# Optimization experiments

Hardware: AMD Instinct MI355X
Metric: run time of the kernel (lower is better)

Reference implementation:

```python
import jax, jax.numpy as jnp
import numpy as np

OBS_LEN = 8
PRED_LEN = 12
BATCH = 65536
EMB = 64
H = 64


def setup_inputs() -> dict:
    key = jax.random.key(0)
    ks = jax.random.split(key, 18)
    s = 1.0 / np.sqrt(H)  # torch default uniform bound scale, used as std here

    def p(k, shape):
        return (jax.random.normal(k, shape, dtype=jnp.float32) * s).astype(jnp.float32)

    return {
        "obs_traj": jax.random.normal(ks[0], (OBS_LEN, BATCH, 2), dtype=jnp.float32),
        "obs_traj_rel": jax.random.normal(ks[1], (OBS_LEN, BATCH, 2), dtype=jnp.float32),
        # encoder params
        "enc_emb_w": p(ks[2], (EMB, 2)),
        "enc_emb_b": p(ks[3], (EMB,)),
        "enc_w_ih": p(ks[4], (4 * H, EMB)),
        "enc_w_hh": p(ks[5], (4 * H, H)),
        "enc_b_ih": p(ks[6], (4 * H,)),
        "enc_b_hh": p(ks[7], (4 * H,)),
        # decoder params
        "dec_emb_w": p(ks[8], (EMB, 2)),
        "dec_emb_b": p(ks[9], (EMB,)),
        "dec_w_ih": p(ks[10], (4 * H, EMB)),
        "dec_w_hh": p(ks[11], (4 * H, H)),
        "dec_b_ih": p(ks[12], (4 * H,)),
        "dec_b_hh": p(ks[13], (4 * H,)),
        "h2p_w": p(ks[14], (2, H)),
        "h2p_b": p(ks[15], (2,)),
    }


def _lstm_cell(h, c, x, w_ih, w_hh, b_ih, b_hh):
    # torch nn.LSTM gate order: i, f, g, o
    gates = x @ w_ih.T + h @ w_hh.T + (b_ih + b_hh)
    i, f, g, o = jnp.split(gates, 4, axis=-1)
    c_new = jax.nn.sigmoid(f) * c + jax.nn.sigmoid(i) * jnp.tanh(g)
    h_new = jax.nn.sigmoid(o) * jnp.tanh(c_new)
    return h_new, c_new


def reference(obs_traj, obs_traj_rel,
              enc_emb_w, enc_emb_b, enc_w_ih, enc_w_hh, enc_b_ih, enc_b_hh,
              dec_emb_w, dec_emb_b, dec_w_ih, dec_w_hh, dec_b_ih, dec_b_hh,
              h2p_w, h2p_b):
    batch = obs_traj_rel.shape[1]

    # ---------- Encoder ----------
    enc_in = obs_traj_rel @ enc_emb_w.T + enc_emb_b  # [T, B, EMB]

    def enc_step(carry, x_t):
        h, c = carry
        h, c = _lstm_cell(h, c, x_t, enc_w_ih, enc_w_hh, enc_b_ih, enc_b_hh)
        return (h, c), None

    h0 = jnp.zeros((batch, H), dtype=obs_traj_rel.dtype)
    c0 = jnp.zeros((batch, H), dtype=obs_traj_rel.dtype)
    (h_enc, _), _ = jax.lax.scan(enc_step, (h0, c0), enc_in)

    # ---------- Decoder ----------
    dec_h = h_enc                                   # final encoder hidden seeds decoder
    dec_c = jnp.zeros((batch, H), dtype=obs_traj_rel.dtype)
    last_pos_rel = obs_traj_rel[-1]
    dec_in = last_pos_rel @ dec_emb_w.T + dec_emb_b  # [B, EMB]

    def dec_step(carry, _):
        h, c, x = carry
        h, c = _lstm_cell(h, c, x, dec_w_ih, dec_w_hh, dec_b_ih, dec_b_hh)
        rel_pos = h @ h2p_w.T + h2p_b               # [B, 2]
        x_next = rel_pos @ dec_emb_w.T + dec_emb_b  # [B, EMB]
        return (h, c, x_next), rel_pos

    (_, _, _), pred_traj_fake_rel = jax.lax.scan(
        dec_step, (dec_h, dec_c, dec_in), None, length=PRED_LEN)
    return pred_traj_fake_rel  # [PRED_LEN, B, 2]
```

## Files before the change

### kernel.cpp

```cpp
#include <hip/hip_runtime.h>

#define OBS_LEN 8
#define PRED_LEN 12
#define TILE_B 32
#define NTHREADS 256

typedef __attribute__((ext_vector_type(8))) short short8;
typedef __attribute__((ext_vector_type(4))) float floatx4;
typedef __attribute__((ext_vector_type(2))) float floatx2;
typedef __attribute__((ext_vector_type(4))) unsigned short ushortx4;
typedef __attribute__((ext_vector_type(2))) unsigned int u32x2;
typedef unsigned short u16;
typedef unsigned int u32;

#define L2E 1.442695040888963f

__device__ __forceinline__ u16 f2bf(float f) {
  __bf16 b = (__bf16)f;
  return __builtin_bit_cast(u16, b);
}
__device__ __forceinline__ float bf2f(u16 h) {
  return __builtin_bit_cast(float, ((u32)h) << 16);
}
__device__ __forceinline__ float rndbf(float f) { return (float)(__bf16)f; }

#if __has_builtin(__builtin_amdgcn_exp2f)
__device__ __forceinline__ float fexp2_(float x) { return __builtin_amdgcn_exp2f(x); }
#else
__device__ __forceinline__ float fexp2_(float x) { return exp2f(x); }
#endif
__device__ __forceinline__ floatx2 exp2v(floatx2 x) {
  floatx2 r;
  r.x = fexp2_(x.x);
  r.y = fexp2_(x.y);
  return r;
}
#if __has_builtin(__builtin_amdgcn_rcpf)
__device__ __forceinline__ floatx2 rcp2(floatx2 x) {
  floatx2 r;
  r.x = __builtin_amdgcn_rcpf(x.x);
  r.y = __builtin_amdgcn_rcpf(x.y);
  return r;
}
#else
__device__ __forceinline__ floatx2 rcp2(floatx2 x) {
  return floatx2{1.0f / x.x, 1.0f / x.y};
}
#endif

__device__ __forceinline__ floatx4 mfma_bf(short8 a, short8 b, floatx4 c) {
  return __builtin_amdgcn_mfma_f32_16x16x32_bf16(a, b, c, 0, 0, 0);
}

__device__ __forceinline__ int swz(int s, int b) {
  return s * 64 + ((b ^ (s & 7)) * 8);
}

__device__ __forceinline__ void load_afrags(const float* __restrict__ W,
                                            short8 (&af)[4][2],
                                            int u0, int q, int l16) {
#pragma unroll
  for (int t = 0; t < 4; ++t)
#pragma unroll
    for (int kf = 0; kf < 2; ++kf) {
      const float* src = W + (t * 64 + u0 + l16) * 64 + kf * 32 + q * 8;
      const floatx4 w0 = *(const floatx4*)src;
      const floatx4 w1 = *(const floatx4*)(src + 4);
      short8 a;
#pragma unroll
      for (int j = 0; j < 4; ++j) {
        a[j] = (short)f2bf(w0[j]);
        a[j + 4] = (short)f2bf(w1[j]);
      }
      af[t][kf] = a;
    }
}

__device__ __forceinline__ void cell_step(const u16* __restrict__ rdh,
                                          const u16* __restrict__ rdx,
                                          u16* __restrict__ wrh,
                                          const short8 (&afh)[4][2],
                                          const short8 (&afx)[4][2],
                                          const float* __restrict__ biasrow,
                                          floatx2 (&c)[2][2],
                                          int q, int l16, int wv, int u0) {
#pragma unroll
  for (int n = 0; n < 2; ++n) {
    const int s = n * 16 + l16;
    const int sw = s & 7;
    const u16* hr = rdh + s * 64;
    const u16* xr = rdx + s * 64;
    const short8 hb0 = *(const short8*)(hr + ((q ^ sw) * 8));
    const short8 hb1 = *(const short8*)(hr + (((q + 4) ^ sw) * 8));
    const short8 xb0 = *(const short8*)(xr + ((q ^ sw) * 8));
    const short8 xb1 = *(const short8*)(xr + (((q + 4) ^ sw) * 8));
    floatx4 acc[4];
#pragma unroll
    for (int t = 0; t < 4; ++t) {
      const floatx4 bias = *(const floatx4*)(biasrow + t * 64 + u0 + q * 4);
      acc[t] = mfma_bf(afh[t][0], hb0, bias);
    }
#pragma unroll
    for (int t = 0; t < 4; ++t) acc[t] = mfma_bf(afx[t][0], xb0, acc[t]);
#pragma unroll
    for (int t = 0; t < 4; ++t) acc[t] = mfma_bf(afh[t][1], hb1, acc[t]);
#pragma unroll
    for (int t = 0; t < 4; ++t) acc[t] = mfma_bf(afx[t][1], xb1, acc[t]);
    u32 hpk[2];
#pragma unroll
    for (int p = 0; p < 2; ++p) {
      const floatx2 iv = {acc[0][2 * p], acc[0][2 * p + 1]};
      const floatx2 fv = {acc[1][2 * p], acc[1][2 * p + 1]};
      const floatx2 gv = {acc[2][2 * p], acc[2][2 * p + 1]};
      const floatx2 ov = {acc[3][2 * p], acc[3][2 * p + 1]};
      const floatx2 ei = exp2v(iv * -L2E);
      const floatx2 ef = exp2v(fv * -L2E);
      const floatx2 eg = exp2v(gv * (2.0f * L2E));
      const floatx2 eo = exp2v(ov * -L2E);
      const floatx2 A = ei + 1.0f;
      const floatx2 F = ef + 1.0f;
      const floatx2 Bg = eg + 1.0f;
      const floatx2 P = A * Bg;
      const floatx2 num = c[n][p] * P + (eg - 1.0f) * F;
      const floatx2 cn = num * rcp2(F * P);
      c[n][p] = cn;
      const floatx2 ec = exp2v(cn * (2.0f * L2E));
      const floatx2 h = (ec - 1.0f) * rcp2((eo + 1.0f) * (ec + 1.0f));
      hpk[p] = (u32)f2bf(h.x) | ((u32)f2bf(h.y) << 16);
    }
    *(u32x2*)(wrh + s * 64 + (((wv * 2 + (q >> 1)) ^ sw) * 8) + (q & 1) * 4) =
        u32x2{hpk[0], hpk[1]};
  }
}

__device__ __forceinline__ void xgen8(float rb0, float rb1,
                                      const float* __restrict__ ew0,
                                      const float* __restrict__ ew1,
                                      const float* __restrict__ eb,
                                      u16* __restrict__ xw, int s8, int p8) {
  short8 v;
#pragma unroll
  for (int j = 0; j < 8; ++j) {
    const int e = p8 * 8 + j;
    v[j] = (short)f2bf(rb0 * ew0[e] + (rb1 * ew1[e] + eb[e]));
  }
  *(short8*)(xw + swz(s8, p8)) = v;
}

__device__ __forceinline__ void areldot(const u16* __restrict__ h,
                                        const floatx2* __restrict__ hwp,
                                        float b2p0, float b2p1, int s8, int p8,
                                        float& r0, float& r1) {
  const short8 hv = *(const short8*)(h + swz(s8, p8));
  floatx2 d = {0.f, 0.f};
#pragma unroll
  for (int j = 0; j < 8; ++j) d = hwp[p8 * 8 + j] * bf2f((u16)hv[j]) + d;
  d.x += __shfl_xor(d.x, 1);
  d.x += __shfl_xor(d.x, 2);
  d.x += __shfl_xor(d.x, 4);
  d.y += __shfl_xor(d.y, 1);
  d.y += __shfl_xor(d.y, 2);
  d.y += __shfl_xor(d.y, 4);
  r0 = d.x + b2p0;
  r1 = d.y + b2p1;
}

__global__ void __launch_bounds__(NTHREADS, 3)
lstm_kernel(const float* __restrict__ obs_rel,
            const float* __restrict__ enc_emb_w, const float* __restrict__ enc_emb_b,
            const float* __restrict__ enc_w_ih, const float* __restrict__ enc_w_hh,
            const float* __restrict__ enc_b_ih, const float* __restrict__ enc_b_hh,
            const float* __restrict__ dec_emb_w, const float* __restrict__ dec_emb_b,
            const float* __restrict__ dec_w_ih, const float* __restrict__ dec_w_hh,
            const float* __restrict__ dec_b_ih, const float* __restrict__ dec_b_hh,
            const float* __restrict__ h2p_w, const float* __restrict__ h2p_b,
            float* __restrict__ out, int batch) {
  __shared__ __align__(16) u16 hS[2][TILE_B * 64];
  __shared__ __align__(16) u16 xS[2][TILE_B * 64];
  __shared__ __align__(16) float posS[OBS_LEN][TILE_B * 2];
  __shared__ __align__(16) float biasS[2][256];
  __shared__ float ew0e[64], ew1e[64], ebe[64];
  __shared__ float ew0d[64], ew1d[64], ebd[64];
  __shared__ __align__(8) floatx2 hwp[64];

  const int tid = threadIdx.x;
  const int wv = tid >> 6, lane = tid & 63;
  const int q = lane >> 4, l16 = lane & 15;
  const int u0 = wv << 4;
  const int s8 = tid >> 3, p8 = tid & 7;
  const long S0 = (long)blockIdx.x * TILE_B;

  if (tid < 128) {
    const int t = tid >> 4, i = tid & 15;
    *(floatx4*)&posS[t][i * 4] =
        *(const floatx4*)(obs_rel + (long)t * batch * 2 + S0 * 2 + i * 4);
  }
  if (tid < 64) {
    ew0e[tid] = rndbf(enc_emb_w[tid * 2]);
    ew1e[tid] = rndbf(enc_emb_w[tid * 2 + 1]);
    ebe[tid] = enc_emb_b[tid];
    ew0d[tid] = rndbf(dec_emb_w[tid * 2]);
    ew1d[tid] = rndbf(dec_emb_w[tid * 2 + 1]);
    ebd[tid] = dec_emb_b[tid];
    hwp[tid] = floatx2{rndbf(h2p_w[tid]), rndbf(h2p_w[64 + tid])};
  }
  biasS[0][tid] = enc_b_ih[tid] + enc_b_hh[tid];
  biasS[1][tid] = dec_b_ih[tid] + dec_b_hh[tid];
  for (int i = tid; i < TILE_B * 64 / 2; i += NTHREADS) ((u32*)&hS[0][0])[i] = 0;

  short8 afh[4][2], afx[4][2];
  floatx2 c[2][2];
  load_afrags(enc_w_hh, afh, u0, q, l16);
  load_afrags(enc_w_ih, afx, u0, q, l16);
  c[0][0] = c[0][1] = c[1][0] = c[1][1] = floatx2{0.f, 0.f};
  const float b2p0 = h2p_b[0], b2p1 = h2p_b[1];
  __syncthreads();
  {
    const floatx2 rr = *(const floatx2*)(&posS[0][s8 * 2]);
    xgen8(rndbf(rr.x), rndbf(rr.y), ew0e, ew1e, ebe, xS[0], s8, p8);
  }
  __syncthreads();

  int pb = 0;
#pragma unroll 1
  for (int t = 0; t < OBS_LEN; ++t) {
    const int tn = t + 1;
    const floatx2 rr = *(const floatx2*)(&posS[(tn < 8) ? tn : 7][s8 * 2]);
    if (tn < 8)
      xgen8(rndbf(rr.x), rndbf(rr.y), ew0e, ew1e, ebe, xS[tn & 1], s8, p8);
    else
      xgen8(rndbf(rr.x), rndbf(rr.y), ew0d, ew1d, ebd, xS[0], s8, p8);
    cell_step(hS[pb], xS[t & 1], hS[pb ^ 1], afh, afx, &biasS[0][0], c,
              q, l16, wv, u0);
    __syncthreads();
    pb ^= 1;
  }

  load_afrags(dec_w_hh, afh, u0, q, l16);
  load_afrags(dec_w_ih, afx, u0, q, l16);
  c[0][0] = c[0][1] = c[1][0] = c[1][1] = floatx2{0.f, 0.f};
  cell_step(hS[pb], xS[0], hS[pb ^ 1], afh, afx, &biasS[1][0], c,
            q, l16, wv, u0);
  __syncthreads();
  pb ^= 1;

#pragma unroll 1
  for (int j = 1; j < PRED_LEN; ++j) {
    float r0, r1;
    areldot(hS[pb], hwp, b2p0, b2p1, s8, p8, r0, r1);
    if (p8 == 0)
      *(floatx2*)(out + (long)(j - 1) * batch * 2 + (S0 + s8) * 2) = floatx2{r0, r1};
    xgen8(rndbf(r0), rndbf(r1), ew0d, ew1d, ebd, xS[0], s8, p8);
    __syncthreads();
    cell_step(hS[pb], xS[0], hS[pb ^ 1], afh, afx, &biasS[1][0], c,
              q, l16, wv, u0);
    __syncthreads();
    pb ^= 1;
  }

  {
    float r0, r1;
    areldot(hS[pb], hwp, b2p0, b2p1, s8, p8, r0, r1);
    if (p8 == 0)
      *(floatx2*)(out + (long)(PRED_LEN - 1) * batch * 2 + (S0 + s8) * 2) =
          floatx2{r0, r1};
  }
}

extern "C" void kernel_launch(void* const* d_in, const int* in_sizes, int n_in,
                              void* d_out, int out_size, void* d_ws, size_t ws_size,
                              hipStream_t stream) {
  const float* obs_rel = (const float*)d_in[1];
  const int batch = in_sizes[1] / (OBS_LEN * 2);

  const int blocks = batch / TILE_B;
  hipLaunchKernelGGL(lstm_kernel, dim3(blocks), dim3(NTHREADS), 0, stream,
                     obs_rel,
                     (const float*)d_in[2], (const float*)d_in[3],
                     (const float*)d_in[4], (const float*)d_in[5],
                     (const float*)d_in[6], (const float*)d_in[7],
                     (const float*)d_in[8], (const float*)d_in[9],
                     (const float*)d_in[10], (const float*)d_in[11],
                     (const float*)d_in[12], (const float*)d_in[13],
                     (const float*)d_in[14], (const float*)d_in[15],
                     (float*)d_out, batch);
}
```

Baseline: 226.4 us.

## Fold decoder h2p and embedding into effective recurrent weights

In the decoder, the next input is a linear function of h (h -> rel_pos -> embedding -> w_ih), so the change folds W_ih·emb·h2p into an effective W_hh and adjusts the bias. Each decoder step then needs half the MFMAs, with no x-generation and one fewer barrier. The rel_pos output is computed from registers in the same step. The trade-off is that intermediate bf16 rounding of rel_pos and x is dropped and the folded weights are rounded to bf16, which changes numerics slightly.

```diff
diff --git a/kernel.cpp b/kernel.cpp
--- a/kernel.cpp
+++ b/kernel.cpp
@@ -8,7 +8,6 @@
 typedef __attribute__((ext_vector_type(8))) short short8;
 typedef __attribute__((ext_vector_type(4))) float floatx4;
 typedef __attribute__((ext_vector_type(2))) float floatx2;
-typedef __attribute__((ext_vector_type(4))) unsigned short ushortx4;
 typedef __attribute__((ext_vector_type(2))) unsigned int u32x2;
 typedef unsigned short u16;
 typedef unsigned int u32;
@@ -76,6 +75,69 @@
     }
 }
 
+__device__ __forceinline__ void load_afrags_eff(const float* __restrict__ Whh,
+                                                const float* __restrict__ aS0,
+                                                const float* __restrict__ aS1,
+                                                const float* __restrict__ hw0,
+                                                const float* __restrict__ hw1,
+                                                short8 (&af)[4][2],
+                                                int u0, int q, int l16) {
+#pragma unroll
+  for (int t = 0; t < 4; ++t) {
+    const int g = t * 64 + u0 + l16;
+    const float a0 = aS0[g], a1 = aS1[g];
+#pragma unroll
+    for (int kf = 0; kf < 2; ++kf) {
+      const int u = kf * 32 + q * 8;
+      const float* src = Whh + g * 64 + u;
+      const floatx4 w0 = *(const floatx4*)src;
+      const floatx4 w1 = *(const floatx4*)(src + 4);
+      const floatx4 p00 = *(const floatx4*)(hw0 + u);
+      const floatx4 p01 = *(const floatx4*)(hw0 + u + 4);
+      const floatx4 p10 = *(const floatx4*)(hw1 + u);
+      const floatx4 p11 = *(const floatx4*)(hw1 + u + 4);
+      short8 a;
+#pragma unroll
+      for (int j = 0; j < 4; ++j) {
+        a[j] = (short)f2bf(w0[j] + a0 * p00[j] + a1 * p10[j]);
+        a[j + 4] = (short)f2bf(w1[j] + a0 * p01[j] + a1 * p11[j]);
+      }
+      af[t][kf] = a;
+    }
+  }
+}
+
+__device__ __forceinline__ void nonlin_store(const floatx4 (&acc)[4],
+                                             floatx2 (&c2)[2],
+                                             u16* __restrict__ wrh,
+                                             int s, int q, int wv) {
+  const int sw = s & 7;
+  u32 hpk[2];
+#pragma unroll
+  for (int p = 0; p < 2; ++p) {
+    const floatx2 iv = {acc[0][2 * p], acc[0][2 * p + 1]};
+    const floatx2 fv = {acc[1][2 * p], acc[1][2 * p + 1]};
+    const floatx2 gv = {acc[2][2 * p], acc[2][2 * p + 1]};
+    const floatx2 ov = {acc[3][2 * p], acc[3][2 * p + 1]};
+    const floatx2 ei = exp2v(iv * -L2E);
+    const floatx2 ef = exp2v(fv * -L2E);
+    const floatx2 eg = exp2v(gv * (2.0f * L2E));
+    const floatx2 eo = exp2v(ov * -L2E);
+    const floatx2 A = ei + 1.0f;
+    const floatx2 F = ef + 1.0f;
+    const floatx2 Bg = eg + 1.0f;
+    const floatx2 P = A * Bg;
+    const floatx2 num = c2[p] * P + (eg - 1.0f) * F;
+    const floatx2 cn = num * rcp2(F * P);
+    c2[p] = cn;
+    const floatx2 ec = exp2v(cn * (2.0f * L2E));
+    const floatx2 h = (ec - 1.0f) * rcp2((eo + 1.0f) * (ec + 1.0f));
+    hpk[p] = (u32)f2bf(h.x) | ((u32)f2bf(h.y) << 16);
+  }
+  *(u32x2*)(wrh + s * 64 + (((wv * 2 + (q >> 1)) ^ sw) * 8) + (q & 1) * 4) =
+      u32x2{hpk[0], hpk[1]};
+}
+
 __device__ __forceinline__ void cell_step(const u16* __restrict__ rdh,
                                           const u16* __restrict__ rdx,
                                           u16* __restrict__ wrh,
@@ -106,30 +168,116 @@
     for (int t = 0; t < 4; ++t) acc[t] = mfma_bf(afh[t][1], hb1, acc[t]);
 #pragma unroll
     for (int t = 0; t < 4; ++t) acc[t] = mfma_bf(afx[t][1], xb1, acc[t]);
-    u32 hpk[2];
-#pragma unroll
-    for (int p = 0; p < 2; ++p) {
-      const floatx2 iv = {acc[0][2 * p], acc[0][2 * p + 1]};
-      const floatx2 fv = {acc[1][2 * p], acc[1][2 * p + 1]};
-      const floatx2 gv = {acc[2][2 * p], acc[2][2 * p + 1]};
-      const floatx2 ov = {acc[3][2 * p], acc[3][2 * p + 1]};
-      const floatx2 ei = exp2v(iv * -L2E);
-      const floatx2 ef = exp2v(fv * -L2E);
-      const floatx2 eg = exp2v(gv * (2.0f * L2E));
-      const floatx2 eo = exp2v(ov * -L2E);
-      const floatx2 A = ei + 1.0f;
-      const floatx2 F = ef + 1.0f;
-      const floatx2 Bg = eg + 1.0f;
-      const floatx2 P = A * Bg;
-      const floatx2 num = c[n][p] * P + (eg - 1.0f) * F;
-      const floatx2 cn = num * rcp2(F * P);
-      c[n][p] = cn;
-      const floatx2 ec = exp2v(cn * (2.0f * L2E));
-      const floatx2 h = (ec - 1.0f) * rcp2((eo + 1.0f) * (ec + 1.0f));
-      hpk[p] = (u32)f2bf(h.x) | ((u32)f2bf(h.y) << 16);
-    }
-    *(u32x2*)(wrh + s * 64 + (((wv * 2 + (q >> 1)) ^ sw) * 8) + (q & 1) * 4) =
-        u32x2{hpk[0], hpk[1]};
+    nonlin_store(acc, c[n], wrh, s, q, wv);
+  }
+}
+
+__device__ __forceinline__ void dec_step_folded(
+    const u16* __restrict__ rdh, u16* __restrict__ wrh,
+    const short8 (&af)[4][2], const float* __restrict__ biasrow,
+    const float* __restrict__ hw0, const float* __restrict__ hw1,
+    float b2p0, float b2p1, float* __restrict__ outp, long S0,
+    floatx2 (&c)[2][2], int q, int l16, int wv, int u0) {
+  short8 hb0[2], hb1[2];
+#pragma unroll
+  for (int n = 0; n < 2; ++n) {
+    const int s = n * 16 + l16, sw = s & 7;
+    const u16* hr = rdh + s * 64;
+    hb0[n] = *(const short8*)(hr + ((q ^ sw) * 8));
+    hb1[n] = *(const short8*)(hr + (((q + 4) ^ sw) * 8));
+  }
+  floatx4 acc[2][4];
+#pragma unroll
+  for (int t = 0; t < 4; ++t) {
+    const floatx4 bias = *(const floatx4*)(biasrow + t * 64 + u0 + q * 4);
+    acc[0][t] = mfma_bf(af[t][0], hb0[0], bias);
+    acc[1][t] = mfma_bf(af[t][0], hb0[1], bias);
+  }
+#pragma unroll
+  for (int t = 0; t < 4; ++t) {
+    acc[0][t] = mfma_bf(af[t][1], hb1[0], acc[0][t]);
+    acc[1][t] = mfma_bf(af[t][1], hb1[1], acc[1][t]);
+  }
+  floatx2 d[2] = {floatx2{0.f, 0.f}, floatx2{0.f, 0.f}};
+#pragma unroll
+  for (int hf = 0; hf < 2; ++hf) {
+    const int ub = hf * 32 + q * 8;
+    const floatx4 wa0 = *(const floatx4*)(hw0 + ub);
+    const floatx4 wa1 = *(const floatx4*)(hw0 + ub + 4);
+    const floatx4 wb0 = *(const floatx4*)(hw1 + ub);
+    const floatx4 wb1 = *(const floatx4*)(hw1 + ub + 4);
+#pragma unroll
+    for (int n = 0; n < 2; ++n) {
+      const short8 hb = hf ? hb1[n] : hb0[n];
+#pragma unroll
+      for (int j = 0; j < 4; ++j) {
+        const float h0 = bf2f((u16)hb[j]);
+        const float h1 = bf2f((u16)hb[j + 4]);
+        d[n].x += wa0[j] * h0 + wa1[j] * h1;
+        d[n].y += wb0[j] * h0 + wb1[j] * h1;
+      }
+    }
+  }
+#pragma unroll
+  for (int n = 0; n < 2; ++n) {
+    d[n].x += __shfl_xor(d[n].x, 16);
+    d[n].x += __shfl_xor(d[n].x, 32);
+    d[n].y += __shfl_xor(d[n].y, 16);
+    d[n].y += __shfl_xor(d[n].y, 32);
+  }
+  if (q == 0) {
+#pragma unroll
+    for (int n = 0; n < 2; ++n)
+      *(floatx2*)(outp + (S0 + n * 16 + l16) * 2) =
+          floatx2{d[n].x + b2p0, d[n].y + b2p1};
+  }
+#pragma unroll
+  for (int n = 0; n < 2; ++n)
+    nonlin_store(acc[n], c[n], wrh, n * 16 + l16, q, wv);
+}
+
+__device__ __forceinline__ void rel_only(const u16* __restrict__ rdh,
+                                         const float* __restrict__ hw0,
+                                         const float* __restrict__ hw1,
+                                         float b2p0, float b2p1,
+                                         float* __restrict__ outp, long S0,
+                                         int q, int l16) {
+  floatx2 d[2] = {floatx2{0.f, 0.f}, floatx2{0.f, 0.f}};
+#pragma unroll
+  for (int n = 0; n < 2; ++n) {
+    const int s = n * 16 + l16, sw = s & 7;
+    const u16* hr = rdh + s * 64;
+    const short8 hb0 = *(const short8*)(hr + ((q ^ sw) * 8));
+    const short8 hb1 = *(const short8*)(hr + (((q + 4) ^ sw) * 8));
+#pragma unroll
+    for (int hf = 0; hf < 2; ++hf) {
+      const int ub = hf * 32 + q * 8;
+      const floatx4 wa0 = *(const floatx4*)(hw0 + ub);
+      const floatx4 wa1 = *(const floatx4*)(hw0 + ub + 4);
+      const floatx4 wb0 = *(const floatx4*)(hw1 + ub);
+      const floatx4 wb1 = *(const floatx4*)(hw1 + ub + 4);
+      const short8 hb = hf ? hb1 : hb0;
+#pragma unroll
+      for (int j = 0; j < 4; ++j) {
+        const float h0 = bf2f((u16)hb[j]);
+        const float h1 = bf2f((u16)hb[j + 4]);
+        d[n].x += wa0[j] * h0 + wa1[j] * h1;
+        d[n].y += wb0[j] * h0 + wb1[j] * h1;
+      }
+    }
+  }
+#pragma unroll
+  for (int n = 0; n < 2; ++n) {
+    d[n].x += __shfl_xor(d[n].x, 16);
+    d[n].x += __shfl_xor(d[n].x, 32);
+    d[n].y += __shfl_xor(d[n].y, 16);
+    d[n].y += __shfl_xor(d[n].y, 32);
+  }
+  if (q == 0) {
+#pragma unroll
+    for (int n = 0; n < 2; ++n)
+      *(floatx2*)(outp + (S0 + n * 16 + l16) * 2) =
+          floatx2{d[n].x + b2p0, d[n].y + b2p1};
   }
 }
 
@@ -145,24 +293,6 @@
     v[j] = (short)f2bf(rb0 * ew0[e] + (rb1 * ew1[e] + eb[e]));
   }
   *(short8*)(xw + swz(s8, p8)) = v;
-}
-
-__device__ __forceinline__ void areldot(const u16* __restrict__ h,
-                                        const floatx2* __restrict__ hwp,
-                                        float b2p0, float b2p1, int s8, int p8,
-                                        float& r0, float& r1) {
-  const short8 hv = *(const short8*)(h + swz(s8, p8));
-  floatx2 d = {0.f, 0.f};
-#pragma unroll
-  for (int j = 0; j < 8; ++j) d = hwp[p8 * 8 + j] * bf2f((u16)hv[j]) + d;
-  d.x += __shfl_xor(d.x, 1);
-  d.x += __shfl_xor(d.x, 2);
-  d.x += __shfl_xor(d.x, 4);
-  d.y += __shfl_xor(d.y, 1);
-  d.y += __shfl_xor(d.y, 2);
-  d.y += __shfl_xor(d.y, 4);
-  r0 = d.x + b2p0;
-  r1 = d.y + b2p1;
 }
 
 __global__ void __launch_bounds__(NTHREADS, 3)
@@ -178,10 +308,11 @@
   __shared__ __align__(16) u16 hS[2][TILE_B * 64];
   __shared__ __align__(16) u16 xS[2][TILE_B * 64];
   __shared__ __align__(16) float posS[OBS_LEN][TILE_B * 2];
-  __shared__ __align__(16) float biasS[2][256];
+  __shared__ __align__(16) float biasS[3][256];
   __shared__ float ew0e[64], ew1e[64], ebe[64];
   __shared__ float ew0d[64], ew1d[64], ebd[64];
-  __shared__ __align__(8) floatx2 hwp[64];
+  __shared__ __align__(16) float aS0[256], aS1[256];
+  __shared__ __align__(16) float hw0S[64], hw1S[64];
 
   const int tid = threadIdx.x;
   const int wv = tid >> 6, lane = tid & 63;
@@ -202,10 +333,29 @@
     ew0d[tid] = rndbf(dec_emb_w[tid * 2]);
     ew1d[tid] = rndbf(dec_emb_w[tid * 2 + 1]);
     ebd[tid] = dec_emb_b[tid];
-    hwp[tid] = floatx2{rndbf(h2p_w[tid]), rndbf(h2p_w[64 + tid])};
+    hw0S[tid] = h2p_w[tid];
+    hw1S[tid] = h2p_w[64 + tid];
   }
   biasS[0][tid] = enc_b_ih[tid] + enc_b_hh[tid];
-  biasS[1][tid] = dec_b_ih[tid] + dec_b_hh[tid];
+  {
+    float A0 = 0.f, A1 = 0.f, B0 = 0.f;
+    const float* wr = dec_w_ih + tid * 64;
+#pragma unroll
+    for (int e4 = 0; e4 < 16; ++e4) {
+      const floatx4 w = *(const floatx4*)(wr + e4 * 4);
+      const floatx4 m0 = *(const floatx4*)(dec_emb_w + e4 * 8);
+      const floatx4 m1 = *(const floatx4*)(dec_emb_w + e4 * 8 + 4);
+      const floatx4 bb = *(const floatx4*)(dec_emb_b + e4 * 4);
+      A0 += w[0] * m0[0] + w[1] * m0[2] + w[2] * m1[0] + w[3] * m1[2];
+      A1 += w[0] * m0[1] + w[1] * m0[3] + w[2] * m1[1] + w[3] * m1[3];
+      B0 += w[0] * bb[0] + w[1] * bb[1] + w[2] * bb[2] + w[3] * bb[3];
+    }
+    aS0[tid] = A0;
+    aS1[tid] = A1;
+    const float db = dec_b_ih[tid] + dec_b_hh[tid];
+    biasS[1][tid] = db;
+    biasS[2][tid] = db + B0 + A0 * h2p_b[0] + A1 * h2p_b[1];
+  }
   for (int i = tid; i < TILE_B * 64 / 2; i += NTHREADS) ((u32*)&hS[0][0])[i] = 0;
 
   short8 afh[4][2], afx[4][2];
@@ -241,30 +391,21 @@
   c[0][0] = c[0][1] = c[1][0] = c[1][1] = floatx2{0.f, 0.f};
   cell_step(hS[pb], xS[0], hS[pb ^ 1], afh, afx, &biasS[1][0], c,
             q, l16, wv, u0);
+  load_afrags_eff(dec_w_hh, aS0, aS1, hw0S, hw1S, afh, u0, q, l16);
   __syncthreads();
   pb ^= 1;
 
 #pragma unroll 1
   for (int j = 1; j < PRED_LEN; ++j) {
-    float r0, r1;
-    areldot(hS[pb], hwp, b2p0, b2p1, s8, p8, r0, r1);
-    if (p8 == 0)
-      *(floatx2*)(out + (long)(j - 1) * batch * 2 + (S0 + s8) * 2) = floatx2{r0, r1};
-    xgen8(rndbf(r0), rndbf(r1), ew0d, ew1d, ebd, xS[0], s8, p8);
-    __syncthreads();
-    cell_step(hS[pb], xS[0], hS[pb ^ 1], afh, afx, &biasS[1][0], c,
-              q, l16, wv, u0);
+    dec_step_folded(hS[pb], hS[pb ^ 1], afh, &biasS[2][0], hw0S, hw1S,
+                    b2p0, b2p1, out + (long)(j - 1) * batch * 2, S0, c,
+                    q, l16, wv, u0);
     __syncthreads();
     pb ^= 1;
   }
 
-  {
-    float r0, r1;
-    areldot(hS[pb], hwp, b2p0, b2p1, s8, p8, r0, r1);
-    if (p8 == 0)
-      *(floatx2*)(out + (long)(PRED_LEN - 1) * batch * 2 + (S0 + s8) * 2) =
-          floatx2{r0, r1};
-  }
+  rel_only(hS[pb], hw0S, hw1S, b2p0, b2p1,
+           out + (long)(PRED_LEN - 1) * batch * 2, S0, q, l16);
 }
 
 extern "C" void kernel_launch(void* const* d_in, const int* in_sizes, int n_in,
```

After: 233.0 us. 1.03x slower.
